# Kernel tuning notes

Hardware: AMD Instinct MI355X
Metric: run time of the kernel (lower is better)

The kernel has to match this reference:

```python
import jax, jax.numpy as jnp
import numpy as np

BLOCK = 32          # MX block size along the contraction dim
E4M3_MAX = 448.0    # max finite magnitude of float8_e4m3fn
E4M3_MAX_EXP = 8.0  # floor(log2(448)) = 8


def mxfp8_quant_dequant(t):
    """Simulate MXFP8 (OCP MX spec): per-32-block E8M0 power-of-two scale,
    elements cast to float8_e4m3fn, then dequantized back to fp32."""
    orig_shape = t.shape
    tb = t.reshape(-1, BLOCK)
    amax = jnp.max(jnp.abs(tb), axis=-1, keepdims=True)
    # E8M0 shared scale: 2^(floor(log2(amax)) - emax_e4m3)
    exp = jnp.floor(jnp.log2(jnp.maximum(amax, 2.0 ** -126))) - E4M3_MAX_EXP
    scale = jnp.exp2(exp)
    q = jnp.clip(tb / scale, -E4M3_MAX, E4M3_MAX)
    q = q.astype(jnp.float8_e4m3fn).astype(t.dtype)  # round-to-nearest fp8
    return (q * scale).reshape(orig_shape)


def setup_inputs() -> dict:
    key = jax.random.key(0)
    k1, k2, k3 = jax.random.split(key, 3)
    B, S, D_IN, D_OUT = 4, 4096, 4096, 4096
    x = jax.random.normal(k1, (B, S, D_IN), dtype=jnp.float32)
    weight = jax.random.normal(k2, (D_OUT, D_IN), dtype=jnp.float32) * 0.02
    bias = jax.random.normal(k3, (D_OUT,), dtype=jnp.float32) * 0.02
    return {"x": x, "weight": weight, "bias": bias}


def reference(x, weight, bias):
    B, S, D_IN = x.shape
    # Inline activation quantization to MXFP8 (blocks of 32 along in_features)
    x2 = x.reshape(-1, D_IN)                 # [B*S, D_IN]
    x_dq = mxfp8_quant_dequant(x2)
    # Weight is stored MXFP8-quantized; dequantize with its block scales
    w_dq = mxfp8_quant_dequant(weight)       # [D_OUT, D_IN]
    out = jnp.einsum('nk,ok->no', x_dq, w_dq) + bias  # microscaled GEMM
    return out.reshape(B, S, -1)
```

## Files before the change

### kernel.cpp

```cpp
#include <hip/hip_runtime.h>
#include <hip/hip_bf16.h>
#include <stdint.h>

typedef __attribute__((ext_vector_type(8))) short bf16x8;
typedef __attribute__((ext_vector_type(4))) float f32x4;
typedef __attribute__((ext_vector_type(8))) unsigned short u16x8;

#define BM 256
#define BN 128
#define BKT 64
#define ABYTES (BM * BKT * 2)
#define BBYTES (BN * BKT * 2)
#define BUFBYTES (ABYTES + BBYTES)
#define NBUF 3

__device__ __forceinline__ float mx_qd_elem(float x, int e) {
    float xs = ldexpf(x, -e);
    xs = fminf(448.f, fmaxf(-448.f, xs));
    float a = fabsf(xs);
    float r;
    if (a < 0.015625f) {
        r = ldexpf(rintf(ldexpf(a, 9)), -9);
    } else {
        int E = (int)((__float_as_uint(a) >> 23) & 0xFF) - 127;
        r = ldexpf(rintf(ldexpf(a, 3 - E)), E - 3);
    }
    r = copysignf(r, xs);
    return ldexpf(r, e);
}

__global__ __launch_bounds__(256) void mx_quant_bf16(
    const float* __restrict__ in, uint16_t* __restrict__ out, int nblk) {
    int t = blockIdx.x * 256 + threadIdx.x;
    if (t >= nblk) return;
    const float4* p = (const float4*)(in + (size_t)t * 32);
    float v[32];
#pragma unroll
    for (int i = 0; i < 8; ++i) {
        float4 fv = p[i];
        v[4 * i + 0] = fv.x; v[4 * i + 1] = fv.y;
        v[4 * i + 2] = fv.z; v[4 * i + 3] = fv.w;
    }
    float amax = 0.f;
#pragma unroll
    for (int i = 0; i < 32; ++i) amax = fmaxf(amax, fabsf(v[i]));
    amax = fmaxf(amax, 1.17549435e-38f);
    int e = (int)((__float_as_uint(amax) >> 23) & 0xFF) - 127 - 8;

    unsigned short res[32];
#pragma unroll
    for (int i = 0; i < 32; ++i) {
        float d = mx_qd_elem(v[i], e);
        res[i] = (unsigned short)(__float_as_uint(d) >> 16);
    }
    u16x8* o = (u16x8*)(out + (size_t)t * 32);
#pragma unroll
    for (int j = 0; j < 4; ++j) {
        u16x8 pack;
#pragma unroll
        for (int i = 0; i < 8; ++i) pack[i] = res[8 * j + i];
        o[j] = pack;
    }
}

#define GLOAD(srcp, ldsoff)                                                     \
    __builtin_amdgcn_global_load_lds(                                           \
        (const __attribute__((address_space(1))) void*)(srcp),                  \
        (__attribute__((address_space(3))) void*)&lds[ldsoff], 16, 0, 0)

__global__ __launch_bounds__(512, 2) void gemm_pipe_bf16(
    const uint16_t* __restrict__ A, const uint16_t* __restrict__ B,
    const float* __restrict__ bias, float* __restrict__ C,
    int Nrows, int K, int O) {
    __shared__ __align__(16) uint8_t lds[NBUF * BUFBYTES];

    const int tid  = threadIdx.x;
    const int lane = tid & 63;
    const int w    = tid >> 6;
    const int f    = lane & 15, g = lane >> 4;
    const int wm   = w >> 1,    wn = w & 1;

    const int nwg  = gridDim.x * gridDim.y;
    const int flat = blockIdx.y * gridDim.x + blockIdx.x;
    const int swz  = (flat & 7) * (nwg >> 3) + (flat >> 3);
    const int bx   = swz % gridDim.x, by = swz / gridDim.x;
    const int rowBase = by * BM, colBase = bx * BN;

    const int rl   = lane >> 3;
    const int scol = ((lane & 7) * 16) ^ ((rl & 7) << 4);
    const uint8_t* gA = (const uint8_t*)A;
    const uint8_t* gB = (const uint8_t*)B;
    const size_t K2 = (size_t)K * 2;

    int aoff[4][2], boff[4][2];
#pragma unroll
    for (int kk = 0; kk < 2; ++kk) {
        int colb = (kk * 64 + g * 16) ^ ((f & 7) << 4);
#pragma unroll
        for (int m = 0; m < 4; ++m)
            aoff[m][kk] = (wm * 64 + m * 16 + f) * 128 + colb;
#pragma unroll
        for (int n = 0; n < 4; ++n)
            boff[n][kk] = ABYTES + (wn * 64 + n * 16 + f) * 128 + colb;
    }

    f32x4 acc[4][4];
#pragma unroll
    for (int m = 0; m < 4; ++m)
#pragma unroll
        for (int n = 0; n < 4; ++n)
#pragma unroll
            for (int j = 0; j < 4; ++j) acc[m][n][j] = 0.f;

    const int nt = K / BKT;

#define STAGE_A(t, li) do {                                                     \
        int _buf = (t) % NBUF;                                                  \
        int _row = (li) * 64 + w * 8 + rl;                                      \
        GLOAD(gA + (size_t)(rowBase + _row) * K2 + (size_t)(t) * (BKT*2) + scol,\
              _buf * BUFBYTES + (li) * 8192 + w * 1024);                        \
    } while (0)
#define STAGE_B(t, li) do {                                                     \
        int _buf = (t) % NBUF;                                                  \
        int _row = (li) * 64 + w * 8 + rl;                                      \
        GLOAD(gB + (size_t)(colBase + _row) * K2 + (size_t)(t) * (BKT*2) + scol,\
              _buf * BUFBYTES + ABYTES + (li) * 8192 + w * 1024);               \
    } while (0)

    STAGE_A(0, 0); STAGE_A(0, 1); STAGE_A(0, 2); STAGE_A(0, 3);
    STAGE_B(0, 0); STAGE_B(0, 1);
    STAGE_A(1, 0); STAGE_A(1, 1); STAGE_A(1, 2); STAGE_A(1, 3);
    STAGE_B(1, 0); STAGE_B(1, 1);
    asm volatile("s_waitcnt vmcnt(6)" ::: "memory");
    __builtin_amdgcn_sched_barrier(0);
    __builtin_amdgcn_s_barrier();
    __builtin_amdgcn_sched_barrier(0);

    for (int t = 0; t < nt; ++t) {
        if (t > 0) {
            if (t == nt - 1) asm volatile("s_waitcnt vmcnt(0)" ::: "memory");
            else             asm volatile("s_waitcnt vmcnt(6)" ::: "memory");
            __builtin_amdgcn_sched_barrier(0);
            __builtin_amdgcn_s_barrier();
            __builtin_amdgcn_sched_barrier(0);
        }
        const int base = (t % NBUF) * BUFBYTES;
        const bool pf = (t + 2) < nt;
        bf16x8 bfr[4];
#pragma unroll
        for (int p = 0; p < 4; ++p) {
            const int kk = p >> 1, mh = p & 1;
            if (pf) {
                if (p == 0) { STAGE_A(t + 2, 0); STAGE_A(t + 2, 1); }
                if (p == 1) { STAGE_A(t + 2, 2); STAGE_A(t + 2, 3); }
                if (p == 2) { STAGE_B(t + 2, 0); STAGE_B(t + 2, 1); }
            }
            if (mh == 0) {
#pragma unroll
                for (int n = 0; n < 4; ++n)
                    bfr[n] = *(const bf16x8*)&lds[base + boff[n][kk]];
            }
            bf16x8 af0 = *(const bf16x8*)&lds[base + aoff[mh * 2 + 0][kk]];
            bf16x8 af1 = *(const bf16x8*)&lds[base + aoff[mh * 2 + 1][kk]];
            __builtin_amdgcn_s_setprio(1);
#pragma unroll
            for (int n = 0; n < 4; ++n) {
                acc[mh * 2 + 0][n] = __builtin_amdgcn_mfma_f32_16x16x32_bf16(
                    af0, bfr[n], acc[mh * 2 + 0][n], 0, 0, 0);
                acc[mh * 2 + 1][n] = __builtin_amdgcn_mfma_f32_16x16x32_bf16(
                    af1, bfr[n], acc[mh * 2 + 1][n], 0, 0, 0);
            }
            __builtin_amdgcn_s_setprio(0);
            __builtin_amdgcn_s_barrier();
            __builtin_amdgcn_sched_barrier(0);
        }
    }

    const int qr = g * 4;
#pragma unroll
    for (int n = 0; n < 4; ++n) {
        int col = colBase + wn * 64 + n * 16 + f;
        float bv = bias[col];
#pragma unroll
        for (int m = 0; m < 4; ++m) {
            int r0 = rowBase + wm * 64 + m * 16 + qr;
#pragma unroll
            for (int j = 0; j < 4; ++j)
                C[(size_t)(r0 + j) * O + col] = acc[m][n][j] + bv;
        }
    }
#undef STAGE_A
#undef STAGE_B
}

extern "C" void kernel_launch(void* const* d_in, const int* in_sizes, int n_in,
                              void* d_out, int out_size, void* d_ws, size_t ws_size,
                              hipStream_t stream) {
    const float* x    = (const float*)d_in[0];
    const float* wgt  = (const float*)d_in[1];
    const float* bias = (const float*)d_in[2];
    float* out = (float*)d_out;

    const int D_OUT = in_sizes[2];
    const int D_IN  = in_sizes[1] / D_OUT;
    const int NROWS = in_sizes[0] / D_IN;

    uint16_t* xq = (uint16_t*)d_ws;
    uint16_t* wq = xq + (size_t)NROWS * D_IN;

    int nblkx = NROWS * (D_IN / 32);
    int nblkw = D_OUT * (D_IN / 32);
    mx_quant_bf16<<<dim3((nblkx + 255) / 256), dim3(256), 0, stream>>>(x, xq, nblkx);
    mx_quant_bf16<<<dim3((nblkw + 255) / 256), dim3(256), 0, stream>>>(wgt, wq, nblkw);

    dim3 grid(D_OUT / BN, NROWS / BM);
    gemm_pipe_bf16<<<grid, dim3(512), 0, stream>>>(xq, wq, bias, out,
                                                   NROWS, D_IN, D_OUT);
}
```

Measured before the change: 723.5 us.

## Enlarge GEMM tile to 256x256 with simpler double-buffered pipeline

Doubles the N tile so each workgroup computes a 256x256 output block, with waves arranged 2x4 and each wave holding 8x4 MFMA accumulators. This raises arithmetic intensity per LDS/global byte. It also replaces the triple-buffered, split-phase prefetch with a plain two-buffer scheme that issues the whole next tile up front and waits for vmcnt(0) at the end of each iteration. Costs are more accumulator registers (128 VGPRs of accumulators), which may hurt occupancy at 2 blocks per CU, and less latency hiding from the shallower pipeline.

```diff
diff --git a/kernel.cpp b/kernel.cpp
--- a/kernel.cpp
+++ b/kernel.cpp
@@ -7,12 +7,11 @@
 typedef __attribute__((ext_vector_type(8))) unsigned short u16x8;
 
 #define BM 256
-#define BN 128
+#define BN 256
 #define BKT 64
 #define ABYTES (BM * BKT * 2)
 #define BBYTES (BN * BKT * 2)
 #define BUFBYTES (ABYTES + BBYTES)
-#define NBUF 3
 
 __device__ __forceinline__ float mx_qd_elem(float x, int e) {
     float xs = ldexpf(x, -e);
@@ -68,17 +67,17 @@
         (const __attribute__((address_space(1))) void*)(srcp),                  \
         (__attribute__((address_space(3))) void*)&lds[ldsoff], 16, 0, 0)
 
-__global__ __launch_bounds__(512, 2) void gemm_pipe_bf16(
+__global__ __launch_bounds__(512, 2) void gemm_256_bf16(
     const uint16_t* __restrict__ A, const uint16_t* __restrict__ B,
     const float* __restrict__ bias, float* __restrict__ C,
     int Nrows, int K, int O) {
-    __shared__ __align__(16) uint8_t lds[NBUF * BUFBYTES];
+    __shared__ __align__(16) uint8_t lds[2 * BUFBYTES];
 
     const int tid  = threadIdx.x;
     const int lane = tid & 63;
     const int w    = tid >> 6;
     const int f    = lane & 15, g = lane >> 4;
-    const int wm   = w >> 1,    wn = w & 1;
+    const int wm   = w >> 2,    wn = w & 3;
 
     const int nwg  = gridDim.x * gridDim.y;
     const int flat = blockIdx.y * gridDim.x + blockIdx.x;
@@ -87,26 +86,26 @@
     const int rowBase = by * BM, colBase = bx * BN;
 
     const int rl   = lane >> 3;
-    const int scol = ((lane & 7) * 16) ^ ((rl & 7) << 4);
+    const int scol = ((lane & 7) * 16) ^ (rl << 4);
     const uint8_t* gA = (const uint8_t*)A;
     const uint8_t* gB = (const uint8_t*)B;
     const size_t K2 = (size_t)K * 2;
 
-    int aoff[4][2], boff[4][2];
+    int aoff[8][2], boff[4][2];
 #pragma unroll
     for (int kk = 0; kk < 2; ++kk) {
-        int colb = (kk * 64 + g * 16) ^ ((f & 7) << 4);
-#pragma unroll
-        for (int m = 0; m < 4; ++m)
-            aoff[m][kk] = (wm * 64 + m * 16 + f) * 128 + colb;
+        const int colb = (kk * 64 + g * 16) ^ ((f & 7) << 4);
+#pragma unroll
+        for (int m = 0; m < 8; ++m)
+            aoff[m][kk] = (wm * 128 + m * 16 + f) * 128 + colb;
 #pragma unroll
         for (int n = 0; n < 4; ++n)
             boff[n][kk] = ABYTES + (wn * 64 + n * 16 + f) * 128 + colb;
     }
 
-    f32x4 acc[4][4];
-#pragma unroll
-    for (int m = 0; m < 4; ++m)
+    f32x4 acc[8][4];
+#pragma unroll
+    for (int m = 0; m < 8; ++m)
 #pragma unroll
         for (int n = 0; n < 4; ++n)
 #pragma unroll
@@ -114,67 +113,55 @@
 
     const int nt = K / BKT;
 
-#define STAGE_A(t, li) do {                                                     \
-        int _buf = (t) % NBUF;                                                  \
-        int _row = (li) * 64 + w * 8 + rl;                                      \
-        GLOAD(gA + (size_t)(rowBase + _row) * K2 + (size_t)(t) * (BKT*2) + scol,\
-              _buf * BUFBYTES + (li) * 8192 + w * 1024);                        \
+#define STAGE(t) do {                                                           \
+        const int _buf = ((t) & 1) * BUFBYTES;                                  \
+        const size_t _kb = (size_t)(t) * (BKT * 2);                             \
+        _Pragma("unroll")                                                       \
+        for (int _i = 0; _i < 4; ++_i)                                          \
+            GLOAD(gA + (size_t)(rowBase + _i * 64 + w * 8 + rl) * K2 + _kb + scol, \
+                  _buf + _i * 8192 + w * 1024);                                 \
+        _Pragma("unroll")                                                       \
+        for (int _i = 0; _i < 4; ++_i)                                          \
+            GLOAD(gB + (size_t)(colBase + _i * 64 + w * 8 + rl) * K2 + _kb + scol, \
+                  _buf + ABYTES + _i * 8192 + w * 1024);                        \
     } while (0)
-#define STAGE_B(t, li) do {                                                     \
-        int _buf = (t) % NBUF;                                                  \
-        int _row = (li) * 64 + w * 8 + rl;                                      \
-        GLOAD(gB + (size_t)(colBase + _row) * K2 + (size_t)(t) * (BKT*2) + scol,\
-              _buf * BUFBYTES + ABYTES + (li) * 8192 + w * 1024);               \
-    } while (0)
-
-    STAGE_A(0, 0); STAGE_A(0, 1); STAGE_A(0, 2); STAGE_A(0, 3);
-    STAGE_B(0, 0); STAGE_B(0, 1);
-    STAGE_A(1, 0); STAGE_A(1, 1); STAGE_A(1, 2); STAGE_A(1, 3);
-    STAGE_B(1, 0); STAGE_B(1, 1);
-    asm volatile("s_waitcnt vmcnt(6)" ::: "memory");
+
+    STAGE(0);
+    asm volatile("s_waitcnt vmcnt(0)" ::: "memory");
     __builtin_amdgcn_sched_barrier(0);
     __builtin_amdgcn_s_barrier();
     __builtin_amdgcn_sched_barrier(0);
 
     for (int t = 0; t < nt; ++t) {
-        if (t > 0) {
-            if (t == nt - 1) asm volatile("s_waitcnt vmcnt(0)" ::: "memory");
-            else             asm volatile("s_waitcnt vmcnt(6)" ::: "memory");
-            __builtin_amdgcn_sched_barrier(0);
-            __builtin_amdgcn_s_barrier();
-            __builtin_amdgcn_sched_barrier(0);
+        if (t + 1 < nt) STAGE(t + 1);
+        const int base = (t & 1) * BUFBYTES;
+
+        bf16x8 bfr[4][2];
+#pragma unroll
+        for (int n = 0; n < 4; ++n) {
+            bfr[n][0] = *(const bf16x8*)&lds[base + boff[n][0]];
+            bfr[n][1] = *(const bf16x8*)&lds[base + boff[n][1]];
         }
-        const int base = (t % NBUF) * BUFBYTES;
-        const bool pf = (t + 2) < nt;
-        bf16x8 bfr[4];
-#pragma unroll
-        for (int p = 0; p < 4; ++p) {
-            const int kk = p >> 1, mh = p & 1;
-            if (pf) {
-                if (p == 0) { STAGE_A(t + 2, 0); STAGE_A(t + 2, 1); }
-                if (p == 1) { STAGE_A(t + 2, 2); STAGE_A(t + 2, 3); }
-                if (p == 2) { STAGE_B(t + 2, 0); STAGE_B(t + 2, 1); }
-            }
-            if (mh == 0) {
-#pragma unroll
-                for (int n = 0; n < 4; ++n)
-                    bfr[n] = *(const bf16x8*)&lds[base + boff[n][kk]];
-            }
-            bf16x8 af0 = *(const bf16x8*)&lds[base + aoff[mh * 2 + 0][kk]];
-            bf16x8 af1 = *(const bf16x8*)&lds[base + aoff[mh * 2 + 1][kk]];
+#pragma unroll
+        for (int m = 0; m < 8; ++m) {
+            bf16x8 a0 = *(const bf16x8*)&lds[base + aoff[m][0]];
+            bf16x8 a1 = *(const bf16x8*)&lds[base + aoff[m][1]];
             __builtin_amdgcn_s_setprio(1);
 #pragma unroll
             for (int n = 0; n < 4; ++n) {
-                acc[mh * 2 + 0][n] = __builtin_amdgcn_mfma_f32_16x16x32_bf16(
-                    af0, bfr[n], acc[mh * 2 + 0][n], 0, 0, 0);
-                acc[mh * 2 + 1][n] = __builtin_amdgcn_mfma_f32_16x16x32_bf16(
-                    af1, bfr[n], acc[mh * 2 + 1][n], 0, 0, 0);
+                acc[m][n] = __builtin_amdgcn_mfma_f32_16x16x32_bf16(
+                    a0, bfr[n][0], acc[m][n], 0, 0, 0);
+                acc[m][n] = __builtin_amdgcn_mfma_f32_16x16x32_bf16(
+                    a1, bfr[n][1], acc[m][n], 0, 0, 0);
             }
             __builtin_amdgcn_s_setprio(0);
-            __builtin_amdgcn_s_barrier();
-            __builtin_amdgcn_sched_barrier(0);
         }
-    }
+        asm volatile("s_waitcnt vmcnt(0)" ::: "memory");
+        __builtin_amdgcn_sched_barrier(0);
+        __builtin_amdgcn_s_barrier();
+        __builtin_amdgcn_sched_barrier(0);
+    }
+#undef STAGE
 
     const int qr = g * 4;
 #pragma unroll
@@ -182,15 +169,13 @@
         int col = colBase + wn * 64 + n * 16 + f;
         float bv = bias[col];
 #pragma unroll
-        for (int m = 0; m < 4; ++m) {
-            int r0 = rowBase + wm * 64 + m * 16 + qr;
+        for (int m = 0; m < 8; ++m) {
+            int r0 = rowBase + wm * 128 + m * 16 + qr;
 #pragma unroll
             for (int j = 0; j < 4; ++j)
                 C[(size_t)(r0 + j) * O + col] = acc[m][n][j] + bv;
         }
     }
-#undef STAGE_A
-#undef STAGE_B
 }
 
 extern "C" void kernel_launch(void* const* d_in, const int* in_sizes, int n_in,
@@ -214,6 +199,6 @@
     mx_quant_bf16<<<dim3((nblkw + 255) / 256), dim3(256), 0, stream>>>(wgt, wq, nblkw);
 
     dim3 grid(D_OUT / BN, NROWS / BM);
-    gemm_pipe_bf16<<<grid, dim3(512), 0, stream>>>(xq, wq, bias, out,
-                                                   NROWS, D_IN, D_OUT);
-}
+    gemm_256_bf16<<<grid, dim3(512), 0, stream>>>(xq, wq, bias, out,
+                                                  NROWS, D_IN, D_OUT);
+}
```

New measurement: 607.4 us. -16.0%, faster.
